# Kernel tuning notes

Measured on AMD Instinct MI355X. Metric: run time of the kernel, lower is better.

The kernel has to match this reference:

```python
import jax, jax.numpy as jnp
import numpy as np

K_TOP = 16
TEMP = 1.0
EPS = 1e-9

def setup_inputs() -> dict:
    key = jax.random.key(0)
    k1, k2, k3 = jax.random.split(key, 3)
    B, H, N, D = 4, 8, 2048, 64
    q = jax.random.normal(k1, (B, H, N, D), dtype=jnp.float32)
    k = jax.random.normal(k2, (B, H, N, D), dtype=jnp.float32)
    u = jax.random.uniform(k3, (B, N, N), dtype=jnp.float32)
    return {"q": q, "k": k, "u": u}

def reference(q, k, u):
    # q, k: [B, H, N, D]; u: uniform noise [B, N, N]
    d_head = q.shape[-1]
    scale = 1.0 / jnp.sqrt(jnp.asarray(d_head, dtype=q.dtype))
    # [B, H, N, N] scores, then mean over heads -> [B, N, N]
    attn_scores = jnp.einsum('bhnd,bhmd->bhnm', q, k) * scale
    logits = attn_scores.mean(axis=1)
    gumbel = -jnp.log(-jnp.log(u + EPS) + EPS)
    probs = jax.nn.softmax((logits + gumbel) / TEMP, axis=-1)
    topk_vals = jax.lax.top_k(probs, K_TOP)[0]          # [B, N, K]
    thresh = topk_vals.min(axis=-1, keepdims=True)      # [B, N, 1]
    sparse_mask = (probs >= thresh).astype(probs.dtype)
    return sparse_mask[:, None, :, :]                   # [B, 1, N, N]
```

## Files before the change

kernel.cpp:

```cpp
#include <hip/hip_runtime.h>
#include <math.h>

#define BB 4
#define HH 8
#define NN 2048
#define DD 64
#define KTOP 16
#define CUT_MARGIN 1e-3f

typedef _Float16 half_t;
typedef __attribute__((ext_vector_type(8))) _Float16 half8;
typedef __attribute__((ext_vector_type(4))) float floatx4;

__device__ __forceinline__ void gl_lds16(const half_t* g, half_t* l) {
    __builtin_amdgcn_global_load_lds(
        (const __attribute__((address_space(1))) void*)g,
        (__attribute__((address_space(3))) void*)l, 16, 0, 0);
}

__global__ __launch_bounds__(256) void split_kblock(const float* __restrict__ q,
                                                    const float* __restrict__ kk,
                                                    half_t* __restrict__ qhi,
                                                    half_t* __restrict__ qlo,
                                                    half_t* __restrict__ khi,
                                                    half_t* __restrict__ klo) {
    const int uidx = blockIdx.x * 256 + threadIdx.x;
    const size_t src = (size_t)uidx * 8;
    const int R  = uidx >> 3;
    const int kg = uidx & 7;
    const int bh = R >> 11;
    const int n  = R & 2047;
    const size_t dst = (((size_t)(bh * 2 + (kg >> 2)) << 11) + n) * 32 + (kg & 3) * 8;

    float a[8], b[8];
    *(float4*)&a[0] = *(const float4*)(q + src);
    *(float4*)&a[4] = *(const float4*)(q + src + 4);
    *(float4*)&b[0] = *(const float4*)(kk + src);
    *(float4*)&b[4] = *(const float4*)(kk + src + 4);
    half8 qh, ql, kh, kl;
#pragma unroll
    for (int e = 0; e < 8; ++e) {
        half_t hq = (half_t)a[e];
        half_t hk = (half_t)b[e];
        qh[e] = hq; ql[e] = (half_t)((a[e] - (float)hq) * 2048.0f);
        kh[e] = hk; kl[e] = (half_t)((b[e] - (float)hk) * 2048.0f);
    }
    *(half8*)(qhi + dst) = qh;
    *(half8*)(qlo + dst) = ql;
    *(half8*)(khi + dst) = kh;
    *(half8*)(klo + dst) = kl;
}

__global__ __launch_bounds__(256, 2) void gemm_f16x3(const half_t* __restrict__ qhi,
                                                     const half_t* __restrict__ qlo,
                                                     const half_t* __restrict__ khi,
                                                     const half_t* __restrict__ klo,
                                                     float* __restrict__ L) {
    const int b  = blockIdx.z;
    const int i0 = blockIdx.y * 128;
    const int j0 = blockIdx.x * 128;
    const int tid  = threadIdx.x;
    const int wave = __builtin_amdgcn_readfirstlane(tid >> 6);
    const int lane = tid & 63;
    const int wr = wave >> 1, wc = wave & 1;
    const int lm = lane & 15, quad = lane >> 4;

    __shared__ __align__(16) half_t Ah[2][4096];
    __shared__ __align__(16) half_t Al[2][4096];
    __shared__ __align__(16) half_t Bh[2][4096];
    __shared__ __align__(16) half_t Bl[2][4096];

    const half_t* gmat;
    half_t* lmat;
    int rowoff;
    if      (wave == 0) { gmat = qhi; lmat = &Ah[0][0]; rowoff = i0; }
    else if (wave == 1) { gmat = qlo; lmat = &Al[0][0]; rowoff = i0; }
    else if (wave == 2) { gmat = khi; lmat = &Bh[0][0]; rowoff = j0; }
    else                { gmat = klo; lmat = &Bl[0][0]; rowoff = j0; }
    const half_t* glane0 = gmat + (((size_t)(b * HH) * 2) * NN + rowoff) * 32 + lane * 8;

#define STAGE(sv, bufv)                                                       \
    {                                                                         \
        const half_t* gs = glane0 + (size_t)(sv) * (NN * 32);                 \
        half_t* ls = lmat + (bufv) * 4096;                                    \
        _Pragma("unroll") for (int i = 0; i < 8; ++i)                         \
            gl_lds16(gs + i * 512, ls + i * 512);                             \
    }

#define LOADFRAG(bufv)                                                       \
    _Pragma("unroll") for (int t = 0; t < 4; ++t) {                          \
        const int am = wr * 64 + t * 16 + lm;                                \
        const int bm = wc * 64 + t * 16 + lm;                                \
        fah[t] = *(const half8*)&Ah[bufv][am * 32 + quad * 8];               \
        fal[t] = *(const half8*)&Al[bufv][am * 32 + quad * 8];               \
        fbh[t] = *(const half8*)&Bh[bufv][bm * 32 + quad * 8];               \
        fbl[t] = *(const half8*)&Bl[bufv][bm * 32 + quad * 8];               \
    }

#define MFMAS                                                                 \
    {                                                                         \
        __builtin_amdgcn_s_setprio(1);                                        \
        _Pragma("unroll") for (int tr = 0; tr < 4; ++tr)                      \
            _Pragma("unroll") for (int tc = 0; tc < 4; ++tc) {                \
                acc1[tr][tc] = __builtin_amdgcn_mfma_f32_16x16x32_f16(        \
                    fah[tr], fbh[tc], acc1[tr][tc], 0, 0, 0);                 \
                acc2[tr][tc] = __builtin_amdgcn_mfma_f32_16x16x32_f16(        \
                    fah[tr], fbl[tc], acc2[tr][tc], 0, 0, 0);                 \
                acc2[tr][tc] = __builtin_amdgcn_mfma_f32_16x16x32_f16(        \
                    fal[tr], fbh[tc], acc2[tr][tc], 0, 0, 0);                 \
            }                                                                 \
        __builtin_amdgcn_s_setprio(0);                                        \
    }

#define WAITL0 { asm volatile("s_waitcnt lgkmcnt(0)" ::: "memory");           \
                 __builtin_amdgcn_sched_barrier(0); }
#define WAITV8 { asm volatile("s_waitcnt vmcnt(8)" ::: "memory");             \
                 __builtin_amdgcn_sched_barrier(0); }
#define WAITV0 { asm volatile("s_waitcnt vmcnt(0)" ::: "memory");             \
                 __builtin_amdgcn_sched_barrier(0); }
#define BAR    { __builtin_amdgcn_s_barrier();                                \
                 __builtin_amdgcn_sched_barrier(0); }

    floatx4 acc1[4][4], acc2[4][4];
#pragma unroll
    for (int tr = 0; tr < 4; ++tr)
#pragma unroll
        for (int tc = 0; tc < 4; ++tc) {
            acc1[tr][tc] = (floatx4)0.0f;
            acc2[tr][tc] = (floatx4)0.0f;
        }

    half8 fah[4], fal[4], fbh[4], fbl[4];

    STAGE(0, 0);
    STAGE(1, 1);
    WAITV8;
    BAR;

#pragma unroll 2
    for (int s = 0; s < 14; ++s) {
        const int cur = s & 1;
        LOADFRAG(cur);
        WAITL0;
        BAR;
        STAGE(s + 2, cur);
        MFMAS;
        WAITV8;
        BAR;
    }
    LOADFRAG(0);
    WAITL0;
    BAR;
    MFMAS;
    WAITV0;
    BAR;
    LOADFRAG(1);
    WAITL0;
    MFMAS;

#undef STAGE
#undef LOADFRAG
#undef MFMAS
#undef WAITL0
#undef WAITV8
#undef WAITV0
#undef BAR

    const float s1 = 0.015625f;
    const float s2 = 0.015625f / 2048.0f;
#pragma unroll
    for (int tr = 0; tr < 4; ++tr)
#pragma unroll
        for (int r = 0; r < 4; ++r) {
            const int grow = i0 + wr * 64 + tr * 16 + quad * 4 + r;
            float* Lp = L + ((size_t)b * NN + grow) * NN + j0 + wc * 64 + lm;
#pragma unroll
            for (int tc = 0; tc < 4; ++tc)
                Lp[tc * 16] = acc1[tr][tc][r] * s1 + acc2[tr][tc][r] * s2;
        }
}

__device__ __forceinline__ unsigned long long flip64(double x) {
    unsigned long long v = (unsigned long long)__double_as_longlong(x);
    return v ^ ((0ULL - (v >> 63)) | 0x8000000000000000ULL);
}
__device__ __forceinline__ double unflip64(unsigned long long k) {
    unsigned long long v = (k >> 63) ? (k ^ 0x8000000000000000ULL) : ~k;
    return __longlong_as_double((long long)v);
}

__global__ __launch_bounds__(64) void topk_mask(float* __restrict__ LM,
                                                const float* __restrict__ u) {
    const int row  = blockIdx.x;
    const int lane = threadIdx.x;
    float* lrow = LM + (size_t)row * NN;
    const float* urow = u + (size_t)row * NN;

    __shared__ int s_idx[64];

    float z[32];
    unsigned hard = 0;
    float4 lb = *(const float4*)(lrow + lane * 4);
    float4 ub = *(const float4*)(urow + lane * 4);
#pragma unroll
    for (int e = 0; e < 8; ++e) {
        float4 lnx, unx;
        if (e < 7) {
            lnx = *(const float4*)(lrow + (e + 1) * 256 + lane * 4);
            unx = *(const float4*)(urow + (e + 1) * 256 + lane * 4);
        }
        const float* ls = (const float*)&lb;
        const float* us = (const float*)&ub;
#pragma unroll
        for (int s = 0; s < 4; ++s) {
            float w = -__logf(us[s] + 1e-9f);
            z[e * 4 + s] = ls[s] - __logf(w + 1e-9f);
            hard |= (us[s] > 0.999f ? 1u : 0u) << (e * 4 + s);
        }
        lb = lnx; ub = unx;
    }

    float v = z[0];
#pragma unroll
    for (int r = 1; r < 32; ++r) v = fmaxf(v, z[r]);
#pragma unroll
    for (int kS = 2; kS <= 64; kS <<= 1) {
#pragma unroll
        for (int j = kS >> 1; j > 0; j >>= 1) {
            float o = __shfl_xor(v, j, 64);
            bool asc = ((lane & kS) == 0);
            bool lower = ((lane & j) == 0);
            float mn = fminf(v, o), mx = fmaxf(v, o);
            v = (asc == lower) ? mn : mx;
        }
    }
    const float cut = __shfl(v, 48, 64) - CUT_MARGIN;

    int c = 0;
#pragma unroll
    for (int r = 0; r < 32; ++r) {
        bool p = (z[r] >= cut);
        unsigned long long m = __ballot(p);
        if (p) {
            int slot = c + __popcll(m & ((1ULL << lane) - 1ULL));
            if (slot < 64) s_idx[slot] = (r >> 2) * 256 + lane * 4 + (r & 3);
        }
        c += __popcll(m);
    }
    if (c > 64) c = 64;

    unsigned long long key = 0xFFFFFFFFFFFFFFFFULL;
    if (lane < c) {
        int idx = s_idx[lane];
        double uu = (double)urow[idx] + 1e-9;
        double w  = -log(uu);
        double g  = -log(w + 1e-9);
        key = flip64((double)lrow[idx] + g);
    }
#pragma unroll
    for (int kS = 2; kS <= 64; kS <<= 1) {
#pragma unroll
        for (int j = kS >> 1; j > 0; j >>= 1) {
            unsigned long long o = __shfl_xor(key, j, 64);
            bool asc = ((lane & kS) == 0);
            bool lower = ((lane & j) == 0);
            unsigned long long mn = (key < o) ? key : o;
            unsigned long long mx = (key < o) ? o : key;
            key = (asc == lower) ? mn : mx;
        }
    }
    const double thresh = unflip64(__shfl(key, c - KTOP, 64));

    const float t_hi = (float)thresh + 3e-4f;
    const float t_lo = (float)thresh - 3e-4f;
    unsigned bm = hard;
#pragma unroll
    for (int r = 0; r < 32; ++r)
        bm |= ((z[r] <= t_hi && z[r] >= t_lo) ? 1u : 0u) << r;
    while (bm) {
        int t = __builtin_ctz(bm);
        bm &= bm - 1;
        const int idx = (t >> 2) * 256 + lane * 4 + (t & 3);
        double uu = (double)urow[idx] + 1e-9;
        double w  = -log(uu);
        double g  = -log(w + 1e-9);
        double z64 = (double)lrow[idx] + g;
        z[t] = (z64 >= thresh) ? 1.0e30f : -1.0e30f;
    }

#pragma unroll
    for (int e = 0; e < 8; ++e) {
        float o[4];
#pragma unroll
        for (int s = 0; s < 4; ++s)
            o[s] = (z[e * 4 + s] > t_hi) ? 1.0f : 0.0f;
        *(float4*)(lrow + e * 256 + lane * 4) = *(float4*)o;
    }
}

extern "C" void kernel_launch(void* const* d_in, const int* in_sizes, int n_in,
                              void* d_out, int out_size, void* d_ws, size_t ws_size,
                              hipStream_t stream) {
    const float* q = (const float*)d_in[0];
    const float* k = (const float*)d_in[1];
    const float* u = (const float*)d_in[2];
    float* out = (float*)d_out;
    const size_t NQ = (size_t)BB * HH * NN * DD;
    half_t* qhi = (half_t*)d_ws;
    half_t* qlo = qhi + NQ;
    half_t* khi = qlo + NQ;
    half_t* klo = khi + NQ;

    split_kblock<<<(int)(NQ / 8 / 256), 256, 0, stream>>>(q, k, qhi, qlo, khi, klo);

    dim3 grid1(NN / 128, NN / 128, BB);
    gemm_f16x3<<<grid1, 256, 0, stream>>>(qhi, qlo, khi, klo, out);

    topk_mask<<<BB * NN, 64, 0, stream>>>(out, u);
}
```

Baseline: 221.6 us.

## Swizzle f16 split layout to avoid LDS bank conflicts; pack 4 topk rows per block

The split kernel now writes Q/K hi/lo halves in a tiled, row-interleaved layout. The GEMM's direct global-to-LDS loads then land each 128-row tile contiguously, and fragment reads use a swizzled index meant to reduce LDS bank conflicts. Separately, the top-k mask kernel processes four rows per 256-thread block instead of one row per 64-thread block, with per-wave shared index buffers. This is meant to cut block launch overhead and improve occupancy.

Result: no change. 218.3 us (-1.5%).

```diff
diff --git a/kernel.cpp b/kernel.cpp
--- a/kernel.cpp
+++ b/kernel.cpp
@@ -18,19 +18,24 @@
         (__attribute__((address_space(3))) void*)l, 16, 0, 0);
 }
 
-__global__ __launch_bounds__(256) void split_kblock(const float* __restrict__ q,
-                                                    const float* __restrict__ kk,
-                                                    half_t* __restrict__ qhi,
-                                                    half_t* __restrict__ qlo,
-                                                    half_t* __restrict__ khi,
-                                                    half_t* __restrict__ klo) {
+__global__ __launch_bounds__(256) void split_swz(const float* __restrict__ q,
+                                                 const float* __restrict__ kk,
+                                                 half_t* __restrict__ qhi,
+                                                 half_t* __restrict__ qlo,
+                                                 half_t* __restrict__ khi,
+                                                 half_t* __restrict__ klo) {
     const int uidx = blockIdx.x * 256 + threadIdx.x;
     const size_t src = (size_t)uidx * 8;
-    const int R  = uidx >> 3;
-    const int kg = uidx & 7;
-    const int bh = R >> 11;
-    const int n  = R & 2047;
-    const size_t dst = (((size_t)(bh * 2 + (kg >> 2)) << 11) + n) * 32 + (kg & 3) * 8;
+    const int R   = uidx >> 3;
+    const int kg8 = uidx & 7;
+    const int bh  = R >> 11;
+    const int n   = R & 2047;
+    const int kb  = kg8 >> 2;
+    const int kgw = kg8 & 3;
+    const int tile = n >> 7;
+    const int r    = n & 127;
+    const int p    = ((r >> 3) << 5) + (kgw << 3) + (r & 7);
+    const size_t dst = (((size_t)(bh * 2 + kb) * 16 + tile) * 512 + p) * 8;
 
     float a[8], b[8];
     *(float4*)&a[0] = *(const float4*)(q + src);
@@ -72,29 +77,31 @@
 
     const half_t* gmat;
     half_t* lmat;
-    int rowoff;
-    if      (wave == 0) { gmat = qhi; lmat = &Ah[0][0]; rowoff = i0; }
-    else if (wave == 1) { gmat = qlo; lmat = &Al[0][0]; rowoff = i0; }
-    else if (wave == 2) { gmat = khi; lmat = &Bh[0][0]; rowoff = j0; }
-    else                { gmat = klo; lmat = &Bl[0][0]; rowoff = j0; }
-    const half_t* glane0 = gmat + (((size_t)(b * HH) * 2) * NN + rowoff) * 32 + lane * 8;
+    int tileoff;
+    if      (wave == 0) { gmat = qhi; lmat = &Ah[0][0]; tileoff = (i0 >> 7) * 4096; }
+    else if (wave == 1) { gmat = qlo; lmat = &Al[0][0]; tileoff = (i0 >> 7) * 4096; }
+    else if (wave == 2) { gmat = khi; lmat = &Bh[0][0]; tileoff = (j0 >> 7) * 4096; }
+    else                { gmat = klo; lmat = &Bl[0][0]; tileoff = (j0 >> 7) * 4096; }
+    const half_t* glane0 = gmat + (size_t)(b * 16) * 65536 + tileoff + lane * 8;
 
 #define STAGE(sv, bufv)                                                       \
     {                                                                         \
-        const half_t* gs = glane0 + (size_t)(sv) * (NN * 32);                 \
+        const half_t* gs = glane0 + (size_t)(sv) * 65536;                     \
         half_t* ls = lmat + (bufv) * 4096;                                    \
         _Pragma("unroll") for (int i = 0; i < 8; ++i)                         \
             gl_lds16(gs + i * 512, ls + i * 512);                             \
     }
 
-#define LOADFRAG(bufv)                                                       \
-    _Pragma("unroll") for (int t = 0; t < 4; ++t) {                          \
-        const int am = wr * 64 + t * 16 + lm;                                \
-        const int bm = wc * 64 + t * 16 + lm;                                \
-        fah[t] = *(const half8*)&Ah[bufv][am * 32 + quad * 8];               \
-        fal[t] = *(const half8*)&Al[bufv][am * 32 + quad * 8];               \
-        fbh[t] = *(const half8*)&Bh[bufv][bm * 32 + quad * 8];               \
-        fbl[t] = *(const half8*)&Bl[bufv][bm * 32 + quad * 8];               \
+#define LOADFRAG(bufv)                                                        \
+    _Pragma("unroll") for (int t = 0; t < 4; ++t) {                           \
+        const int am = wr * 64 + t * 16 + lm;                                 \
+        const int bm = wc * 64 + t * 16 + lm;                                 \
+        const int ai = ((am >> 3) << 8) + (quad << 6) + ((am & 7) << 3);      \
+        const int bi = ((bm >> 3) << 8) + (quad << 6) + ((bm & 7) << 3);      \
+        fah[t] = *(const half8*)&Ah[bufv][ai];                                \
+        fal[t] = *(const half8*)&Al[bufv][ai];                                \
+        fbh[t] = *(const half8*)&Bh[bufv][bi];                                \
+        fbl[t] = *(const half8*)&Bl[bufv][bi];                                \
     }
 
 #define MFMAS                                                                 \
@@ -189,14 +196,15 @@
     return __longlong_as_double((long long)v);
 }
 
-__global__ __launch_bounds__(64) void topk_mask(float* __restrict__ LM,
-                                                const float* __restrict__ u) {
-    const int row  = blockIdx.x;
-    const int lane = threadIdx.x;
+__global__ __launch_bounds__(256) void topk_mask(float* __restrict__ LM,
+                                                 const float* __restrict__ u) {
+    const int wave = threadIdx.x >> 6;
+    const int lane = threadIdx.x & 63;
+    const int row  = blockIdx.x * 4 + wave;
     float* lrow = LM + (size_t)row * NN;
     const float* urow = u + (size_t)row * NN;
 
-    __shared__ int s_idx[64];
+    __shared__ int s_idx[4][64];
 
     float z[32];
     unsigned hard = 0;
@@ -243,7 +251,7 @@
         unsigned long long m = __ballot(p);
         if (p) {
             int slot = c + __popcll(m & ((1ULL << lane) - 1ULL));
-            if (slot < 64) s_idx[slot] = (r >> 2) * 256 + lane * 4 + (r & 3);
+            if (slot < 64) s_idx[wave][slot] = (r >> 2) * 256 + lane * 4 + (r & 3);
         }
         c += __popcll(m);
     }
@@ -251,7 +259,7 @@
 
     unsigned long long key = 0xFFFFFFFFFFFFFFFFULL;
     if (lane < c) {
-        int idx = s_idx[lane];
+        int idx = s_idx[wave][lane];
         double uu = (double)urow[idx] + 1e-9;
         double w  = -log(uu);
         double g  = -log(w + 1e-9);
@@ -311,10 +319,10 @@
     half_t* khi = qlo + NQ;
     half_t* klo = khi + NQ;
 
-    split_kblock<<<(int)(NQ / 8 / 256), 256, 0, stream>>>(q, k, qhi, qlo, khi, klo);
+    split_swz<<<(int)(NQ / 8 / 256), 256, 0, stream>>>(q, k, qhi, qlo, khi, klo);
 
     dim3 grid1(NN / 128, NN / 128, BB);
     gemm_f16x3<<<grid1, 256, 0, stream>>>(qhi, qlo, khi, klo, out);
 
-    topk_mask<<<BB * NN, 64, 0, stream>>>(out, u);
-}
+    topk_mask<<<BB * NN / 4, 256, 0, stream>>>(out, u);
+}
```
